# Kernel tuning notes

Hardware: AMD Instinct MI355X
Metric: run time of the kernel (lower is better)

## Reference

```python
import jax, jax.numpy as jnp
import numpy as np

N_E = 50000
N_R = 1000
E = 800000
E_HIDDEN = 256
R_HIDDEN = 64
NEG_SLOPE = 0.01  # torch F.leaky_relu default


def segment_softmax(logits, seg, num_segments):
    # numerically stable per-segment softmax over edges
    seg_max = jax.ops.segment_max(logits, seg, num_segments=num_segments)
    seg_max = jnp.where(jnp.isfinite(seg_max), seg_max, 0.0)
    ex = jnp.exp(logits - seg_max[seg])
    denom = jax.ops.segment_sum(ex, seg, num_segments=num_segments)
    return ex / (denom[seg] + 1e-16)


def setup_inputs() -> dict:
    key = jax.random.key(0)
    ks = jax.random.split(key, 9)
    return {
        "x_e": jax.random.normal(ks[0], (N_E, E_HIDDEN), dtype=jnp.float32),
        "x_r": jax.random.normal(ks[1], (N_R, R_HIDDEN), dtype=jnp.float32),
        "edge_index": jax.random.randint(ks[2], (2, E), 0, N_E, dtype=jnp.int64),
        "rel": jax.random.randint(ks[3], (E,), 0, N_R, dtype=jnp.int64),
        "line_graph_index": jax.random.randint(ks[4], (2, E), 0, E, dtype=jnp.int64),
        "line_graph_val": jax.random.uniform(ks[5], (E,), dtype=jnp.float32),
        "a_h_w": jax.random.normal(ks[6], (E_HIDDEN,), dtype=jnp.float32),
        "a_t_w": jax.random.normal(ks[7], (E_HIDDEN,), dtype=jnp.float32),
        "a_r_w": jax.random.normal(ks[8], (R_HIDDEN,), dtype=jnp.float32),
    }


def reference(x_e, x_r, edge_index, rel, line_graph_index, line_graph_val, a_h_w, a_t_w, a_r_w):
    head, tail = edge_index[0], edge_index[1]
    # per-node scalar scores, gathered per edge
    s_e_h = jnp.einsum("nd,d->n", x_e, a_h_w)  # [N_e]
    s_e_t = jnp.einsum("nd,d->n", x_e, a_t_w)  # [N_e]
    s_r = jnp.einsum("rd,d->r", x_r, a_r_w)    # [N_r]
    e_h = s_e_h[head]
    e_t = s_e_t[tail]
    e_r = s_r[rel]

    n_e = x_e.shape[0]
    msg = x_r[rel]  # [E, r_hidden]

    # head branch: segment softmax over head groups, scatter-aggregate x_r[rel]
    alpha_h = segment_softmax(jax.nn.leaky_relu(e_h + e_r, NEG_SLOPE), head, n_e)
    x_e_h = jax.ops.segment_sum(alpha_h[:, None] * msg, head, num_segments=n_e)

    # tail branch: softmax grouped by tail, but spmm still scatters into head rows
    alpha_t = segment_softmax(jax.nn.leaky_relu(e_t + e_r, NEG_SLOPE), tail, n_e)
    x_e_t = jax.ops.segment_sum(alpha_t[:, None] * msg, tail, num_segments=n_e)

    return jnp.concatenate([x_e_h, x_e_t], axis=1)  # [N_e, 2*r_hidden]
```

## Files before the change

kernel.cpp:

```cpp
#include <hip/hip_runtime.h>

static constexpr int kNE = 50000;
static constexpr int kNR = 1000;
static constexpr int kE  = 800000;
static constexpr int kEH = 256;
static constexpr int kRH = 64;
static constexpr float kNeg = 0.01f;

static constexpr int kSegs = 2 * kNE;
static constexpr int kSegsPerB = 128;
static constexpr int kB = (kSegs + kSegsPerB - 1) / kSegsPerB;
static constexpr int kCap = 3072;
static constexpr int kEdgesPerBin = 2048;
static constexpr int kBinBlocks  = (kE + kEdgesPerBin - 1) / kEdgesPerBin;
static constexpr int kNodeBlocks = kNE / 8;
static constexpr int kRelBlocks  = kNR / 8;

__device__ __forceinline__ float lrelu(float x){ return x > 0.f ? x : kNeg * x; }

__global__ __launch_bounds__(512) void k_bin_scores(
        const float* __restrict__ xe, const float* __restrict__ ahw,
        const float* __restrict__ atw, const float* __restrict__ xr,
        const float* __restrict__ arw,
        const int* __restrict__ head, const int* __restrict__ tail,
        const int* __restrict__ rel,
        float* __restrict__ s_h, float* __restrict__ s_t, float* __restrict__ s_r,
        int* __restrict__ bucket_fill, unsigned int* __restrict__ records){
    __shared__ int cnt[1024];
    __shared__ int start[1024];
    __shared__ int cur[1024];
    __shared__ unsigned int srt[2 * kEdgesPerBin];
    __shared__ int scan_tmp[512];
    __shared__ int sh_total;

    int blk = blockIdx.x;
    int tid = threadIdx.x;
    int lane = tid & 63;

    if (blk >= kBinBlocks){
        int sb = blk - kBinBlocks;
        if (sb < kNodeBlocks){
            int node = sb * 8 + (tid >> 6);
            const float4* row = (const float4*)(xe + (size_t)node * kEH);
            float4 xv = row[lane];
            float4 av = ((const float4*)ahw)[lane];
            float4 bv = ((const float4*)atw)[lane];
            float ph = xv.x*av.x + xv.y*av.y + xv.z*av.z + xv.w*av.w;
            float pt = xv.x*bv.x + xv.y*bv.y + xv.z*bv.z + xv.w*bv.w;
            #pragma unroll
            for (int o = 32; o > 0; o >>= 1){
                ph += __shfl_down(ph, o, 64);
                pt += __shfl_down(pt, o, 64);
            }
            if (lane == 0){ s_h[node] = ph; s_t[node] = pt; }
        } else {
            int r = (sb - kNodeBlocks) * 8 + (tid >> 6);
            float p = xr[(size_t)r * kRH + lane] * arw[lane];
            #pragma unroll
            for (int o = 32; o > 0; o >>= 1) p += __shfl_down(p, o, 64);
            if (lane == 0) s_r[r] = p;
        }
        return;
    }

    int e0 = blk * kEdgesPerBin;
    for (int i = tid; i < 1024; i += 512) cnt[i] = 0;
    __syncthreads();

    unsigned int recs[8];
    #pragma unroll
    for (int p = 0; p < 4; ++p){
        int e = e0 + p * 512 + tid;
        unsigned int rh = 0xFFFFFFFFu, rt = 0xFFFFFFFFu;
        if (e < kE){
            int h = head[e], t = tail[e], r = rel[e];
            rh = ((unsigned int)h << 10) | (unsigned int)r;
            rt = ((unsigned int)(kNE + t) << 10) | (unsigned int)r;
            atomicAdd(&cnt[h >> 7], 1);
            atomicAdd(&cnt[(kNE + t) >> 7], 1);
        }
        recs[p] = rh; recs[4 + p] = rt;
    }
    __syncthreads();

    int c0 = cnt[2 * tid], c1 = cnt[2 * tid + 1];
    int v = c0 + c1;
    scan_tmp[tid] = v;
    __syncthreads();
    for (int o = 1; o < 512; o <<= 1){
        int add = (tid >= o) ? scan_tmp[tid - o] : 0;
        __syncthreads();
        scan_tmp[tid] += add;
        __syncthreads();
    }
    int incl = scan_tmp[tid];
    int base = incl - v;
    start[2 * tid] = base;          cur[2 * tid] = base;
    start[2 * tid + 1] = base + c0; cur[2 * tid + 1] = base + c0;
    if (tid == 511) sh_total = incl;
    __syncthreads();

    #pragma unroll
    for (int p = 0; p < 8; ++p){
        unsigned int rc = recs[p];
        if (rc != 0xFFFFFFFFu){
            int slot = atomicAdd(&cur[rc >> 17], 1);
            srt[slot] = rc;
        }
    }
    __syncthreads();

    for (int i = tid; i < kB; i += 512){
        int c = cur[i] - start[i];
        int gb = (c > 0) ? atomicAdd(&bucket_fill[i], c) : 0;
        cur[i] = gb - start[i];
    }
    __syncthreads();

    int total = sh_total;
    for (int j = tid; j < total; j += 512){
        unsigned int rc = srt[j];
        int bk = rc >> 17;
        int g  = cur[bk] + j;
        if (g < kCap) records[(size_t)bk * kCap + g] = rc;
    }
}

__global__ __launch_bounds__(256) void k_sort_aggregate(
        const int* __restrict__ bucket_fill, const unsigned int* __restrict__ records,
        const float* __restrict__ s_h, const float* __restrict__ s_t,
        const float* __restrict__ s_r, const float* __restrict__ xr,
        float* __restrict__ out){
    __shared__ float srl[kNR];
    __shared__ unsigned short relbuf[kCap];
    __shared__ float alphabuf[kCap];
    __shared__ float invbuf[kSegsPerB];
    __shared__ int cnt[kSegsPerB], start[kSegsPerB], cur[kSegsPerB], scanbuf[kSegsPerB];

    int b = blockIdx.x;
    int tid = threadIdx.x;

    for (int i = tid; i < kNR; i += 256) srl[i] = s_r[i];
    if (tid < kSegsPerB) cnt[tid] = 0;
    __syncthreads();

    int nrec = bucket_fill[b];
    if (nrec > kCap) nrec = kCap;
    const unsigned int* rb = records + (size_t)b * kCap;

    unsigned int recs[12];
    #pragma unroll
    for (int p = 0; p < 12; ++p){
        int idx = p * 256 + tid;
        unsigned int rc = 0xFFFFFFFFu;
        if (idx < nrec){
            rc = rb[idx];
            atomicAdd(&cnt[(rc >> 10) & 127], 1);
        }
        recs[p] = rc;
    }
    __syncthreads();
    if (tid < kSegsPerB) scanbuf[tid] = cnt[tid];
    __syncthreads();
    for (int o = 1; o < kSegsPerB; o <<= 1){
        int v = 0;
        if (tid < kSegsPerB && tid >= o) v = scanbuf[tid - o];
        __syncthreads();
        if (tid < kSegsPerB) scanbuf[tid] += v;
        __syncthreads();
    }
    if (tid < kSegsPerB){
        int s = scanbuf[tid] - cnt[tid];
        start[tid] = s;
        cur[tid] = s;
    }
    __syncthreads();
    #pragma unroll
    for (int p = 0; p < 12; ++p){
        unsigned int rc = recs[p];
        if (rc != 0xFFFFFFFFu){
            int slot = atomicAdd(&cur[(rc >> 10) & 127], 1);
            relbuf[slot] = (unsigned short)(rc & 1023u);
        }
    }
    __syncthreads();

    if (tid < kSegsPerB){
        int gseg = b * kSegsPerB + tid;
        if (gseg < kSegs){
            int deg = cnt[tid], st = start[tid];
            float sn = (gseg < kNE) ? s_h[gseg] : s_t[gseg - kNE];
            float m = -INFINITY;
            for (int k = 0; k < deg; ++k){
                float lg = lrelu(sn + srl[relbuf[st + k]]);
                alphabuf[st + k] = lg;
                m = fmaxf(m, lg);
            }
            float ssum = 0.f;
            for (int k = 0; k < deg; ++k){
                float e = __expf(alphabuf[st + k] - m);
                alphabuf[st + k] = e;
                ssum += e;
            }
            invbuf[tid] = 1.f / (ssum + 1e-16f);
        }
    }
    __syncthreads();

    int grp = tid >> 4;
    int sub = tid & 15;
    for (int ls = grp; ls < kSegsPerB; ls += 16){
        int gseg = b * kSegsPerB + ls;
        if (gseg >= kSegs) break;
        int deg = cnt[ls], st = start[ls];
        float inv = invbuf[ls];
        float4 acc = {0.f, 0.f, 0.f, 0.f};
        int k = 0;
        for (; k + 4 <= deg; k += 4){
            int r0 = relbuf[st + k],     r1 = relbuf[st + k + 1];
            int r2 = relbuf[st + k + 2], r3 = relbuf[st + k + 3];
            float a0 = alphabuf[st + k] * inv,     a1 = alphabuf[st + k + 1] * inv;
            float a2 = alphabuf[st + k + 2] * inv, a3 = alphabuf[st + k + 3] * inv;
            float4 v0 = ((const float4*)(xr + (size_t)r0 * kRH))[sub];
            float4 v1 = ((const float4*)(xr + (size_t)r1 * kRH))[sub];
            float4 v2 = ((const float4*)(xr + (size_t)r2 * kRH))[sub];
            float4 v3 = ((const float4*)(xr + (size_t)r3 * kRH))[sub];
            acc.x += a0*v0.x + a1*v1.x + a2*v2.x + a3*v3.x;
            acc.y += a0*v0.y + a1*v1.y + a2*v2.y + a3*v3.y;
            acc.z += a0*v0.z + a1*v1.z + a2*v2.z + a3*v3.z;
            acc.w += a0*v0.w + a1*v1.w + a2*v2.w + a3*v3.w;
        }
        for (; k < deg; ++k){
            int rr = relbuf[st + k];
            float a = alphabuf[st + k] * inv;
            float4 v = ((const float4*)(xr + (size_t)rr * kRH))[sub];
            acc.x += a*v.x; acc.y += a*v.y; acc.z += a*v.z; acc.w += a*v.w;
        }
        bool isHead = gseg < kNE;
        int node = isHead ? gseg : gseg - kNE;
        float4* op = (float4*)(out + (size_t)node * (2 * kRH) + (isHead ? 0 : kRH));
        op[sub] = acc;
    }
}

extern "C" void kernel_launch(void* const* d_in, const int* in_sizes, int n_in,
                              void* d_out, int out_size, void* d_ws, size_t ws_size,
                              hipStream_t stream) {
    const float* xe  = (const float*)d_in[0];
    const float* xr  = (const float*)d_in[1];
    const int* edge_index = (const int*)d_in[2];
    const int* rel        = (const int*)d_in[3];
    const float* ahw = (const float*)d_in[6];
    const float* atw = (const float*)d_in[7];
    const float* arw = (const float*)d_in[8];
    float* out = (float*)d_out;

    const int* head = edge_index;
    const int* tail = edge_index + kE;

    char* ws = (char*)d_ws;
    float* s_h  = (float*)ws;                    ws += kNE * sizeof(float);
    float* s_t  = (float*)ws;                    ws += kNE * sizeof(float);
    float* s_r  = (float*)ws;                    ws += kNR * sizeof(float);
    int*   bucket_fill = (int*)ws;               ws += kB * sizeof(int);
    unsigned int* records = (unsigned int*)ws;   ws += (size_t)kB * kCap * sizeof(unsigned int);

    hipMemsetAsync(bucket_fill, 0, kB * sizeof(int), stream);
    k_bin_scores<<<kBinBlocks + kNodeBlocks + kRelBlocks, 512, 0, stream>>>(
        xe, ahw, atw, xr, arw, head, tail, rel, s_h, s_t, s_r, bucket_fill, records);
    k_sort_aggregate<<<kB, 256, 0, stream>>>(bucket_fill, records, s_h, s_t, s_r, xr, out);
}
```

Measured before the change: 168.4 us.

## Halve segments per bucket and pack binned records into 16-bit values

Buckets now hold 64 segments instead of 128, so each record needs only a 6-bit local segment id plus a 10-bit relation and fits in an unsigned short. This halves the intermediate records buffer traffic and doubles the number of aggregate blocks for more parallelism. The leaky-relu logit is now computed during the scatter into shared memory, which removes a serial pass from the per-segment softmax thread. The cost is a larger counting histogram (2048 entries) in the binning kernel, a four-way scan per thread, and a per-bucket capacity cap that is now tighter in absolute terms.

Result: no change. 171.7 us (+2.0%).

```diff
diff --git a/kernel.cpp b/kernel.cpp
--- a/kernel.cpp
+++ b/kernel.cpp
@@ -7,14 +7,15 @@
 static constexpr int kRH = 64;
 static constexpr float kNeg = 0.01f;
 
+static constexpr int kSegsPerB = 64;
 static constexpr int kSegs = 2 * kNE;
-static constexpr int kSegsPerB = 128;
 static constexpr int kB = (kSegs + kSegsPerB - 1) / kSegsPerB;
-static constexpr int kCap = 3072;
+static constexpr int kCap = 1536;
 static constexpr int kEdgesPerBin = 2048;
 static constexpr int kBinBlocks  = (kE + kEdgesPerBin - 1) / kEdgesPerBin;
 static constexpr int kNodeBlocks = kNE / 8;
 static constexpr int kRelBlocks  = kNR / 8;
+static constexpr int kCntPad = 2048;
 
 __device__ __forceinline__ float lrelu(float x){ return x > 0.f ? x : kNeg * x; }
 
@@ -25,10 +26,10 @@
         const int* __restrict__ head, const int* __restrict__ tail,
         const int* __restrict__ rel,
         float* __restrict__ s_h, float* __restrict__ s_t, float* __restrict__ s_r,
-        int* __restrict__ bucket_fill, unsigned int* __restrict__ records){
-    __shared__ int cnt[1024];
-    __shared__ int start[1024];
-    __shared__ int cur[1024];
+        int* __restrict__ bucket_fill, unsigned short* __restrict__ records){
+    __shared__ int cnt[kCntPad];
+    __shared__ int start[kCntPad];
+    __shared__ int cur[kCntPad];
     __shared__ unsigned int srt[2 * kEdgesPerBin];
     __shared__ int scan_tmp[512];
     __shared__ int sh_total;
@@ -64,7 +65,7 @@
     }
 
     int e0 = blk * kEdgesPerBin;
-    for (int i = tid; i < 1024; i += 512) cnt[i] = 0;
+    for (int i = tid; i < kCntPad; i += 512) cnt[i] = 0;
     __syncthreads();
 
     unsigned int recs[8];
@@ -76,15 +77,15 @@
             int h = head[e], t = tail[e], r = rel[e];
             rh = ((unsigned int)h << 10) | (unsigned int)r;
             rt = ((unsigned int)(kNE + t) << 10) | (unsigned int)r;
-            atomicAdd(&cnt[h >> 7], 1);
-            atomicAdd(&cnt[(kNE + t) >> 7], 1);
+            atomicAdd(&cnt[rh >> 16], 1);
+            atomicAdd(&cnt[rt >> 16], 1);
         }
         recs[p] = rh; recs[4 + p] = rt;
     }
     __syncthreads();
 
-    int c0 = cnt[2 * tid], c1 = cnt[2 * tid + 1];
-    int v = c0 + c1;
+    int c0 = cnt[4 * tid], c1 = cnt[4 * tid + 1], c2 = cnt[4 * tid + 2], c3 = cnt[4 * tid + 3];
+    int v = c0 + c1 + c2 + c3;
     scan_tmp[tid] = v;
     __syncthreads();
     for (int o = 1; o < 512; o <<= 1){
@@ -95,8 +96,10 @@
     }
     int incl = scan_tmp[tid];
     int base = incl - v;
-    start[2 * tid] = base;          cur[2 * tid] = base;
-    start[2 * tid + 1] = base + c0; cur[2 * tid + 1] = base + c0;
+    start[4 * tid] = base;                cur[4 * tid] = base;
+    start[4 * tid + 1] = base + c0;       cur[4 * tid + 1] = base + c0;
+    start[4 * tid + 2] = base + c0 + c1;  cur[4 * tid + 2] = base + c0 + c1;
+    start[4 * tid + 3] = base + c0 + c1 + c2; cur[4 * tid + 3] = base + c0 + c1 + c2;
     if (tid == 511) sh_total = incl;
     __syncthreads();
 
@@ -104,7 +107,7 @@
     for (int p = 0; p < 8; ++p){
         unsigned int rc = recs[p];
         if (rc != 0xFFFFFFFFu){
-            int slot = atomicAdd(&cur[rc >> 17], 1);
+            int slot = atomicAdd(&cur[rc >> 16], 1);
             srt[slot] = rc;
         }
     }
@@ -120,18 +123,19 @@
     int total = sh_total;
     for (int j = tid; j < total; j += 512){
         unsigned int rc = srt[j];
-        int bk = rc >> 17;
+        int bk = rc >> 16;
         int g  = cur[bk] + j;
-        if (g < kCap) records[(size_t)bk * kCap + g] = rc;
+        if (g < kCap) records[(size_t)bk * kCap + g] = (unsigned short)(rc & 0xFFFFu);
     }
 }
 
 __global__ __launch_bounds__(256) void k_sort_aggregate(
-        const int* __restrict__ bucket_fill, const unsigned int* __restrict__ records,
+        const int* __restrict__ bucket_fill, const unsigned short* __restrict__ records,
         const float* __restrict__ s_h, const float* __restrict__ s_t,
         const float* __restrict__ s_r, const float* __restrict__ xr,
         float* __restrict__ out){
     __shared__ float srl[kNR];
+    __shared__ float sn[kSegsPerB];
     __shared__ unsigned short relbuf[kCap];
     __shared__ float alphabuf[kCap];
     __shared__ float invbuf[kSegsPerB];
@@ -141,21 +145,28 @@
     int tid = threadIdx.x;
 
     for (int i = tid; i < kNR; i += 256) srl[i] = s_r[i];
-    if (tid < kSegsPerB) cnt[tid] = 0;
+    if (tid < kSegsPerB){
+        cnt[tid] = 0;
+        int gseg = b * kSegsPerB + tid;
+        float s = 0.f;
+        if (gseg < kNE) s = s_h[gseg];
+        else if (gseg < kSegs) s = s_t[gseg - kNE];
+        sn[tid] = s;
+    }
     __syncthreads();
 
     int nrec = bucket_fill[b];
     if (nrec > kCap) nrec = kCap;
-    const unsigned int* rb = records + (size_t)b * kCap;
-
-    unsigned int recs[12];
-    #pragma unroll
-    for (int p = 0; p < 12; ++p){
+    const unsigned short* rb = records + (size_t)b * kCap;
+
+    unsigned short recs[6];
+    #pragma unroll
+    for (int p = 0; p < 6; ++p){
         int idx = p * 256 + tid;
-        unsigned int rc = 0xFFFFFFFFu;
+        unsigned short rc = 0xFFFFu;
         if (idx < nrec){
             rc = rb[idx];
-            atomicAdd(&cnt[(rc >> 10) & 127], 1);
+            atomicAdd(&cnt[rc >> 10], 1);
         }
         recs[p] = rc;
     }
@@ -176,34 +187,29 @@
     }
     __syncthreads();
     #pragma unroll
-    for (int p = 0; p < 12; ++p){
-        unsigned int rc = recs[p];
-        if (rc != 0xFFFFFFFFu){
-            int slot = atomicAdd(&cur[(rc >> 10) & 127], 1);
-            relbuf[slot] = (unsigned short)(rc & 1023u);
+    for (int p = 0; p < 6; ++p){
+        unsigned short rc = recs[p];
+        if (rc != 0xFFFFu){
+            int ls = rc >> 10;
+            int rr = rc & 1023;
+            int slot = atomicAdd(&cur[ls], 1);
+            relbuf[slot] = (unsigned short)rr;
+            alphabuf[slot] = lrelu(sn[ls] + srl[rr]);
         }
     }
     __syncthreads();
 
     if (tid < kSegsPerB){
-        int gseg = b * kSegsPerB + tid;
-        if (gseg < kSegs){
-            int deg = cnt[tid], st = start[tid];
-            float sn = (gseg < kNE) ? s_h[gseg] : s_t[gseg - kNE];
-            float m = -INFINITY;
-            for (int k = 0; k < deg; ++k){
-                float lg = lrelu(sn + srl[relbuf[st + k]]);
-                alphabuf[st + k] = lg;
-                m = fmaxf(m, lg);
-            }
-            float ssum = 0.f;
-            for (int k = 0; k < deg; ++k){
-                float e = __expf(alphabuf[st + k] - m);
-                alphabuf[st + k] = e;
-                ssum += e;
-            }
-            invbuf[tid] = 1.f / (ssum + 1e-16f);
-        }
+        int deg = cnt[tid], st = start[tid];
+        float m = -INFINITY;
+        for (int k = 0; k < deg; ++k) m = fmaxf(m, alphabuf[st + k]);
+        float ssum = 0.f;
+        for (int k = 0; k < deg; ++k){
+            float e = __expf(alphabuf[st + k] - m);
+            alphabuf[st + k] = e;
+            ssum += e;
+        }
+        invbuf[tid] = 1.f / (ssum + 1e-16f);
     }
     __syncthreads();
 
@@ -262,8 +268,8 @@
     float* s_h  = (float*)ws;                    ws += kNE * sizeof(float);
     float* s_t  = (float*)ws;                    ws += kNE * sizeof(float);
     float* s_r  = (float*)ws;                    ws += kNR * sizeof(float);
-    int*   bucket_fill = (int*)ws;               ws += kB * sizeof(int);
-    unsigned int* records = (unsigned int*)ws;   ws += (size_t)kB * kCap * sizeof(unsigned int);
+    int*   bucket_fill = (int*)ws;               ws += ((kB + 255) & ~255) * sizeof(int);
+    unsigned short* records = (unsigned short*)ws; ws += (size_t)kB * kCap * sizeof(unsigned short);
 
     hipMemsetAsync(bucket_fill, 0, kB * sizeof(int), stream);
     k_bin_scores<<<kBinBlocks + kNodeBlocks + kRelBlocks, 512, 0, stream>>>(
```
